# Kernel tuning notes

Hardware: AMD Instinct MI355X
Metric: run time of the kernel (lower is better)

## Reference

```python
import jax, jax.numpy as jnp
import numpy as np

S = 8    # number of path-segments
U = 32   # per-segment input width (subscript 'u')
V = 32   # per-segment output width (subscript 'v')
C = 32   # number of weight groups (indexed dimension)
Z = 65536  # number of rows


def setup_inputs() -> dict:
    key = jax.random.key(0)
    k1, k2, k3 = jax.random.split(key, 3)
    input1 = jax.random.normal(k1, (C, S * U * V), dtype=jnp.float32) * 0.05  # grouped weights
    input2 = jax.random.normal(k2, (Z, S * U), dtype=jnp.float32)             # row features
    counts = jnp.full((C,), Z // C, dtype=jnp.int32)                          # rows per group, contiguous
    coefficients = jax.random.uniform(k3, (S,), dtype=jnp.float32, minval=0.5, maxval=1.5)
    return {"input1": input1, "input2": input2, "counts": counts, "coefficients": coefficients}


def reference(input1, input2, counts, coefficients):
    # Segment-indexed grouped linear: rows are contiguous per group (sizes = counts).
    # For each path-segment s: out_s[z, v] = coeff_s * sum_u x_s[z, u] * W_s[g(z), u, v]
    # Final output concatenates the S segment outputs along the last dim.
    seg_ids = jnp.repeat(jnp.arange(C, dtype=jnp.int32), counts, total_repeat_length=Z)  # [Z]
    outs = []
    for s in range(S):
        W = input1[:, s * U * V:(s + 1) * U * V].reshape(C, U, V)  # [C,U,V]
        x = input2[:, s * U:(s + 1) * U]                           # [Z,U]
        Wz = W[seg_ids]                                            # [Z,U,V] gather by group
        outs.append(coefficients[s] * jnp.einsum('zu,zuv->zv', x, Wz))
    return jnp.concatenate(outs, axis=-1)  # [Z, S*V]
```

## Files before the change

### kernel.cpp

```cpp
#include <hip/hip_runtime.h>


constexpr int S = 8, U = 32, V = 32, C = 32, Z = 65536;
constexpr int SU = S * U;
constexpr int SV = S * V;
constexpr int NT = 256;

typedef float  f4    __attribute__((ext_vector_type(4)));
typedef float  f32x16 __attribute__((ext_vector_type(16)));
typedef short  bf16x8 __attribute__((ext_vector_type(8)));

__device__ __forceinline__ short f2bf(float f) {
  unsigned u = __builtin_bit_cast(unsigned, f);
  u = (u + 0x7FFFu + ((u >> 16) & 1u)) >> 16;
  return (short)u;
}

__global__ __launch_bounds__(NT) void IndexedLinear_kernel(
    const float* __restrict__ W_all,
    const float* __restrict__ X,
    const int*   __restrict__ counts,
    const float* __restrict__ coeff,
    float*       __restrict__ out)
{
  const int lane = threadIdx.x & 63;
  const int g    = blockIdx.x * (NT / 64) + (threadIdx.x >> 6);
  const int s    = g & 7;
  const int z0   = (g >> 3) * 32;

  const int m = lane & 31;
  const int h = lane >> 5;

  const float* xr = X + (size_t)(z0 + m) * SU + s * U;
  f4 xa = __builtin_nontemporal_load((const f4*)(xr + 8 * h));
  f4 xb = __builtin_nontemporal_load((const f4*)(xr + 8 * h + 4));
  f4 xc = __builtin_nontemporal_load((const f4*)(xr + 16 + 8 * h));
  f4 xd = __builtin_nontemporal_load((const f4*)(xr + 16 + 8 * h + 4));

  int c = (lane < C) ? counts[lane] : 0;
  int inc = c;
  #pragma unroll
  for (int d = 1; d < 32; d <<= 1) {
    int o = __shfl_up(inc, d, 64);
    if (lane >= d) inc += o;
  }
  const int exc = inc - c;
  const unsigned long long ma = __ballot(lane < C && exc <= z0);
  const unsigned long long mb = __ballot(lane < C && exc <= z0 + 31);
  const int segA = __popcll(ma) - 1;
  const int segB = __popcll(mb) - 1;

  const float cs = coeff[s];

  if (segA == segB) {
    const float* wb = W_all + (size_t)segA * (S * U * V) + s * (U * V);

    bf16x8 b1, b2;
    #pragma unroll
    for (int j = 0; j < 8; ++j)
      b1[j] = f2bf(wb[(8 * h + j) * V + m] * cs);
    #pragma unroll
    for (int j = 0; j < 8; ++j)
      b2[j] = f2bf(wb[(16 + 8 * h + j) * V + m] * cs);

    bf16x8 a1, a2;
    #pragma unroll
    for (int i = 0; i < 4; ++i) {
      a1[i]     = f2bf(xa[i]);
      a1[4 + i] = f2bf(xb[i]);
      a2[i]     = f2bf(xc[i]);
      a2[4 + i] = f2bf(xd[i]);
    }

    f32x16 acc = {};
    acc = __builtin_amdgcn_mfma_f32_32x32x16_bf16(a1, b1, acc, 0, 0, 0);
    acc = __builtin_amdgcn_mfma_f32_32x32x16_bf16(a2, b2, acc, 0, 0, 0);

    float* ob = out + (size_t)z0 * SV + s * V + m;
    #pragma unroll
    for (int r = 0; r < 16; ++r) {
      const int row = (r & 3) + 8 * (r >> 2) + 4 * h;
      __builtin_nontemporal_store(acc[r], ob + (size_t)row * SV);
    }
  } else {
    const int zz = z0 + m;
    int sg = 0;
    #pragma unroll 1
    for (int i = 1; i < C; ++i) {
      const int pi = __shfl(exc, i, 64);
      if (pi <= zz) sg = i;
    }
    const float* wr = W_all + (size_t)sg * (S * U * V) + s * (U * V) + 16 * h;
    const float* xrow = X + (size_t)zz * SU + s * U;
    float accv[16] = {};
    #pragma unroll 1
    for (int u = 0; u < U; ++u) {
      const float xu = xrow[u];
      #pragma unroll
      for (int j = 0; j < 16; ++j) accv[j] += xu * wr[u * V + j];
    }
    float* ob = out + (size_t)zz * SV + s * V + 16 * h;
    #pragma unroll
    for (int j = 0; j < 16; ++j) ob[j] = accv[j] * cs;
  }
}

extern "C" void kernel_launch(void* const* d_in, const int* in_sizes, int n_in,
                              void* d_out, int out_size, void* d_ws, size_t ws_size,
                              hipStream_t stream) {
  const float* input1       = (const float*)d_in[0];
  const float* input2       = (const float*)d_in[1];
  const int*   counts       = (const int*)d_in[2];
  const float* coefficients = (const float*)d_in[3];
  float*       out          = (float*)d_out;

  const int tiles = (Z / 32) * S;
  const int grid  = tiles / (NT / 64);
  IndexedLinear_kernel<<<grid, NT, 0, stream>>>(input1, input2, counts,
                                                coefficients, out);
}
```

Before: 136.3 us.

## Stage X row tile into LDS via async global_load_lds, two segments per wave

Each block now owns 32 rows and covers all 8 segments, with each wave handling two segments. The whole X tile is staged into shared memory with async global-to-LDS loads, and the weight fetch and conversion overlap with those loads before a barrier. This aims for fully coalesced X reads and fewer, larger blocks, at the cost of 32KB LDS per block and a block-wide sync.

```diff
diff --git a/kernel.cpp b/kernel.cpp
--- a/kernel.cpp
+++ b/kernel.cpp
@@ -5,15 +5,23 @@
 constexpr int SU = S * U;
 constexpr int SV = S * V;
 constexpr int NT = 256;
+constexpr int BZ = 32;
 
-typedef float  f4    __attribute__((ext_vector_type(4)));
+typedef float  f4     __attribute__((ext_vector_type(4)));
 typedef float  f32x16 __attribute__((ext_vector_type(16)));
 typedef short  bf16x8 __attribute__((ext_vector_type(8)));
+
+typedef const __attribute__((address_space(1))) unsigned gu32;
+typedef __attribute__((address_space(3))) unsigned lu32;
 
 __device__ __forceinline__ short f2bf(float f) {
   unsigned u = __builtin_bit_cast(unsigned, f);
   u = (u + 0x7FFFu + ((u >> 16) & 1u)) >> 16;
   return (short)u;
+}
+
+__device__ __forceinline__ int xidx(int m, int c) {
+  return ((m >> 3) << 9) + ((c >> 3) << 6) + ((c & 7) << 3) + (m & 7);
 }
 
 __global__ __launch_bounds__(NT) void IndexedLinear_kernel(
@@ -23,64 +31,87 @@
     const float* __restrict__ coeff,
     float*       __restrict__ out)
 {
-  const int lane = threadIdx.x & 63;
-  const int g    = blockIdx.x * (NT / 64) + (threadIdx.x >> 6);
-  const int s    = g & 7;
-  const int z0   = (g >> 3) * 32;
+  const int tid  = threadIdx.x;
+  const int lane = tid & 63;
+  const int w    = tid >> 6;
+  const int z0   = blockIdx.x * BZ;
 
-  const int m = lane & 31;
-  const int h = lane >> 5;
+  __shared__ f4 XL[BZ * 64];
 
-  const float* xr = X + (size_t)(z0 + m) * SU + s * U;
-  f4 xa = __builtin_nontemporal_load((const f4*)(xr + 8 * h));
-  f4 xb = __builtin_nontemporal_load((const f4*)(xr + 8 * h + 4));
-  f4 xc = __builtin_nontemporal_load((const f4*)(xr + 16 + 8 * h));
-  f4 xd = __builtin_nontemporal_load((const f4*)(xr + 16 + 8 * h + 4));
+  {
+    const char* gbase = (const char*)X
+        + (size_t)(z0 + 8 * w + (lane & 7)) * (SU * 4) + (lane >> 3) * 16;
+    #pragma unroll
+    for (int k = 0; k < 8; ++k) {
+      const char* gp = gbase + k * 128;
+      f4* lp = XL + (8 * w + k) * 64;
+      __builtin_amdgcn_global_load_lds((gu32*)gp, (lu32*)lp, 16, 0, 0);
+    }
+  }
 
-  int c = (lane < C) ? counts[lane] : 0;
-  int inc = c;
+  int cnt = (lane < C) ? counts[lane] : 0;
+  int inc = cnt;
   #pragma unroll
   for (int d = 1; d < 32; d <<= 1) {
     int o = __shfl_up(inc, d, 64);
     if (lane >= d) inc += o;
   }
-  const int exc = inc - c;
+  const int exc = inc - cnt;
   const unsigned long long ma = __ballot(lane < C && exc <= z0);
-  const unsigned long long mb = __ballot(lane < C && exc <= z0 + 31);
+  const unsigned long long mb = __ballot(lane < C && exc <= z0 + BZ - 1);
   const int segA = __popcll(ma) - 1;
   const int segB = __popcll(mb) - 1;
+  const bool uni = (segA == segB);
 
-  const float cs = coeff[s];
+  const int m = lane & 31;
+  const int h = lane >> 5;
+  const int s0 = 2 * w;
 
-  if (segA == segB) {
-    const float* wb = W_all + (size_t)segA * (S * U * V) + s * (U * V);
+  bf16x8 b1[2], b2[2];
+  if (uni) {
+    const float* wseg = W_all + (size_t)segA * (S * U * V);
+    #pragma unroll
+    for (int t = 0; t < 2; ++t) {
+      const int s = s0 + t;
+      const float cs = coeff[s];
+      const float* wb = wseg + s * (U * V);
+      #pragma unroll
+      for (int j = 0; j < 8; ++j)
+        b1[t][j] = f2bf(wb[(8 * h + j) * V + m] * cs);
+      #pragma unroll
+      for (int j = 0; j < 8; ++j)
+        b2[t][j] = f2bf(wb[(16 + 8 * h + j) * V + m] * cs);
+    }
+  }
 
-    bf16x8 b1, b2;
+  __syncthreads();
+
+  if (uni) {
     #pragma unroll
-    for (int j = 0; j < 8; ++j)
-      b1[j] = f2bf(wb[(8 * h + j) * V + m] * cs);
-    #pragma unroll
-    for (int j = 0; j < 8; ++j)
-      b2[j] = f2bf(wb[(16 + 8 * h + j) * V + m] * cs);
+    for (int t = 0; t < 2; ++t) {
+      const int s = s0 + t;
+      const f4 xa = XL[xidx(m, s * 8 + 2 * h)];
+      const f4 xb = XL[xidx(m, s * 8 + 2 * h + 1)];
+      const f4 xc = XL[xidx(m, s * 8 + 4 + 2 * h)];
+      const f4 xd = XL[xidx(m, s * 8 + 4 + 2 * h + 1)];
+      bf16x8 a1, a2;
+      #pragma unroll
+      for (int i = 0; i < 4; ++i) {
+        a1[i]     = f2bf(xa[i]);
+        a1[4 + i] = f2bf(xb[i]);
+        a2[i]     = f2bf(xc[i]);
+        a2[4 + i] = f2bf(xd[i]);
+      }
+      f32x16 acc = {};
+      acc = __builtin_amdgcn_mfma_f32_32x32x16_bf16(a1, b1[t], acc, 0, 0, 0);
+      acc = __builtin_amdgcn_mfma_f32_32x32x16_bf16(a2, b2[t], acc, 0, 0, 0);
 
-    bf16x8 a1, a2;
-    #pragma unroll
-    for (int i = 0; i < 4; ++i) {
-      a1[i]     = f2bf(xa[i]);
-      a1[4 + i] = f2bf(xb[i]);
-      a2[i]     = f2bf(xc[i]);
-      a2[4 + i] = f2bf(xd[i]);
-    }
-
-    f32x16 acc = {};
-    acc = __builtin_amdgcn_mfma_f32_32x32x16_bf16(a1, b1, acc, 0, 0, 0);
-    acc = __builtin_amdgcn_mfma_f32_32x32x16_bf16(a2, b2, acc, 0, 0, 0);
-
-    float* ob = out + (size_t)z0 * SV + s * V + m;
-    #pragma unroll
-    for (int r = 0; r < 16; ++r) {
-      const int row = (r & 3) + 8 * (r >> 2) + 4 * h;
-      __builtin_nontemporal_store(acc[r], ob + (size_t)row * SV);
+      float* ob = out + (size_t)z0 * SV + s * V + m;
+      #pragma unroll
+      for (int r = 0; r < 16; ++r) {
+        const int row = (r & 3) + 8 * (r >> 2) + 4 * h;
+        __builtin_nontemporal_store(acc[r], ob + (size_t)row * SV);
+      }
     }
   } else {
     const int zz = z0 + m;
@@ -90,18 +121,27 @@
       const int pi = __shfl(exc, i, 64);
       if (pi <= zz) sg = i;
     }
-    const float* wr = W_all + (size_t)sg * (S * U * V) + s * (U * V) + 16 * h;
-    const float* xrow = X + (size_t)zz * SU + s * U;
-    float accv[16] = {};
     #pragma unroll 1
-    for (int u = 0; u < U; ++u) {
-      const float xu = xrow[u];
+    for (int t = 0; t < 2; ++t) {
+      const int s = s0 + t;
+      const float cs = coeff[s];
+      const float* wr = W_all + (size_t)sg * (S * U * V) + s * (U * V) + 16 * h;
+      float accv[16] = {};
+      #pragma unroll 1
+      for (int cq = 0; cq < 8; ++cq) {
+        const f4 xv = XL[xidx(m, s * 8 + cq)];
+        #pragma unroll
+        for (int ii = 0; ii < 4; ++ii) {
+          const int u = cq * 4 + ii;
+          const float xu = xv[ii];
+          #pragma unroll
+          for (int j = 0; j < 16; ++j) accv[j] += xu * wr[u * V + j];
+        }
+      }
+      float* ob = out + (size_t)zz * SV + s * V + 16 * h;
       #pragma unroll
-      for (int j = 0; j < 16; ++j) accv[j] += xu * wr[u * V + j];
+      for (int j = 0; j < 16; ++j) ob[j] = accv[j] * cs;
     }
-    float* ob = out + (size_t)zz * SV + s * V + 16 * h;
-    #pragma unroll
-    for (int j = 0; j < 16; ++j) ob[j] = accv[j] * cs;
   }
 }
 
@@ -114,8 +154,7 @@
   const float* coefficients = (const float*)d_in[3];
   float*       out          = (float*)d_out;
 
-  const int tiles = (Z / 32) * S;
-  const int grid  = tiles / (NT / 64);
+  const int grid = Z / BZ;
   IndexedLinear_kernel<<<grid, NT, 0, stream>>>(input1, input2, counts,
                                                 coefficients, out);
 }
```

Measured after the change: 117.9 us. 13.5% less time.
